# Kernel optimization log

Measured on AMD Instinct MI355X. Metric: run time of the kernel, lower is better.

Reference implementation:

```python
import jax, jax.numpy as jnp
import numpy as np

N_HEAD = 16
D_MODEL = 1024
HEAD_DIM = D_MODEL // N_HEAD


def setup_inputs() -> dict:
    key = jax.random.key(0)
    ks = jax.random.split(key, 12)
    B, S, D = 2, 2048, D_MODEL
    scale = 1.0 / np.sqrt(D)
    inp = {
        "q": jax.random.normal(ks[0], (B, S, D), jnp.float32),
        "k": jax.random.normal(ks[1], (B, S, D), jnp.float32),
        "v": jax.random.normal(ks[2], (B, S, D), jnp.float32),
        "mask": jax.random.randint(ks[3], (B, 1, S, S), 0, 2, jnp.int32),
        "wq": jax.random.normal(ks[4], (D, D), jnp.float32) * scale,
        "bq": jnp.zeros((D,), jnp.float32),
        "wk": jax.random.normal(ks[5], (D, D), jnp.float32) * scale,
        "bk": jnp.zeros((D,), jnp.float32),
        "wv": jax.random.normal(ks[6], (D, D), jnp.float32) * scale,
        "bv": jnp.zeros((D,), jnp.float32),
        "wo": jax.random.normal(ks[7], (D, D), jnp.float32) * scale,
        "bo": jnp.zeros((D,), jnp.float32),
    }
    return inp


def _split_heads(x):
    B, S, D = x.shape
    return x.reshape(B, S, N_HEAD, HEAD_DIM).transpose(0, 2, 1, 3)  # [B,H,S,Hd]


def reference(q, k, v, mask, wq, bq, wk, bk, wv, bv, wo, bo):
    _q = _split_heads(q @ wq + bq)
    _k = _split_heads(k @ wk + bk)
    _v = _split_heads(v @ wv + bv)
    inv = 1.0 / (jnp.sqrt(jnp.float32(HEAD_DIM)) + 1e-8)
    score = jnp.einsum("bhqd,bhkd->bhqk", _q, _k) * inv
    score = score + mask.astype(score.dtype) * (-1e9)
    attn = jax.nn.softmax(score, axis=-1)
    ctx = jnp.einsum("bhqk,bhkd->bhqd", attn, _v)
    B, H, S, Hd = ctx.shape
    ctx = ctx.transpose(0, 2, 1, 3).reshape(B, S, H * Hd)
    return ctx @ wo + bo  # dropout is identity (eval / drop_rate=0)
```

## Files before the change

### kernel.cpp

```cpp
#include <hip/hip_runtime.h>

typedef unsigned short u16;
typedef __bf16 bf16x8_t __attribute__((ext_vector_type(8)));
typedef float  f32x4_t  __attribute__((ext_vector_type(4)));
typedef u16    us8_t    __attribute__((ext_vector_type(8)));
typedef u16    us4_t    __attribute__((ext_vector_type(4)));

__device__ __forceinline__ u16 f2bf(float f) {
    __bf16 h = (__bf16)f;
    return __builtin_bit_cast(u16, h);
}
__device__ __forceinline__ bf16x8_t ld_bf8(const u16* p) {
    us8_t u = *(const us8_t*)p;
    return __builtin_bit_cast(bf16x8_t, u);
}
__device__ __forceinline__ f32x4_t mfma16(bf16x8_t a, bf16x8_t b, f32x4_t c) {
    return __builtin_amdgcn_mfma_f32_16x16x32_bf16(a, b, c, 0, 0, 0);
}
__device__ __forceinline__ float exp2_fast(float x) {
#if __has_builtin(__builtin_amdgcn_exp2f)
    return __builtin_amdgcn_exp2f(x);
#else
    return exp2f(x);
#endif
}

__device__ __forceinline__ void dma16(const u16* g, u16* l) {
#if __has_builtin(__builtin_amdgcn_global_load_lds)
    __builtin_amdgcn_global_load_lds((const __attribute__((address_space(1))) unsigned int*)(g),
                                     (__attribute__((address_space(3))) unsigned int*)(l), 16, 0, 0);
#else
    *(us8_t*)l = *(const us8_t*)g;
#endif
}

__global__ __launch_bounds__(256) void prep_kernel(
    const float* __restrict__ q, const float* __restrict__ k, const float* __restrict__ v,
    const int* __restrict__ mask,
    const float* __restrict__ w0, const float* __restrict__ w1,
    const float* __restrict__ w2, const float* __restrict__ w3,
    u16* __restrict__ Qc, u16* __restrict__ Kc, u16* __restrict__ Vc,
    u16* __restrict__ Wt, unsigned* __restrict__ mp)
{
    __shared__ u16 t[64][65];
    const int bid = blockIdx.x, tid = threadIdx.x;
    if (bid < 6144) {
        const int z = bid >> 11, x = bid & 2047;
        const float* src = (z == 0) ? q : (z == 1) ? k : v;
        u16* dst = (z == 0) ? Qc : (z == 1) ? Kc : Vc;
        const size_t i = ((size_t)x * 256 + tid) * 8;
        float4 a = *(const float4*)(src + i);
        float4 b = *(const float4*)(src + i + 4);
        us8_t w;
        w[0] = f2bf(a.x); w[1] = f2bf(a.y); w[2] = f2bf(a.z); w[3] = f2bf(a.w);
        w[4] = f2bf(b.x); w[5] = f2bf(b.y); w[6] = f2bf(b.z); w[7] = f2bf(b.w);
        *(us8_t*)(dst + i) = w;
    } else if (bid < 7168) {
        const int r2 = bid - 6144;
        const int z = r2 >> 8, rem = r2 & 255;
        const float* src = (z == 0) ? w0 : (z == 1) ? w1 : (z == 2) ? w2 : w3;
        u16* dst = Wt + (size_t)z * 1048576;
        const int bk = (rem & 15) * 64, bn = (rem >> 4) * 64;
        const int r = tid >> 2, c4 = tid & 3;
        for (int i = 0; i < 4; i++) {
            float4 vv = *(const float4*)(src + (size_t)(bk + r) * 1024 + bn + c4 * 16 + i * 4);
            t[r][c4 * 16 + i * 4 + 0] = f2bf(vv.x);
            t[r][c4 * 16 + i * 4 + 1] = f2bf(vv.y);
            t[r][c4 * 16 + i * 4 + 2] = f2bf(vv.z);
            t[r][c4 * 16 + i * 4 + 3] = f2bf(vv.w);
        }
        __syncthreads();
        for (int i = 0; i < 2; i++) {
            us8_t w;
            for (int j = 0; j < 8; j++) w[j] = t[c4 * 16 + i * 8 + j][r];
            *(us8_t*)(dst + (size_t)(bn + r) * 1024 + bk + c4 * 16 + i * 8) = w;
        }
    } else {
        const int w = (bid - 7168) * 256 + tid;
        const int* src = mask + (size_t)w * 32;
        unsigned bits = 0u;
        for (int i = 0; i < 32; i += 4) {
            int4 vv = *(const int4*)(src + i);
            bits |= (unsigned)(vv.x != 0) << (i + 0);
            bits |= (unsigned)(vv.y != 0) << (i + 1);
            bits |= (unsigned)(vv.z != 0) << (i + 2);
            bits |= (unsigned)(vv.w != 0) << (i + 3);
        }
        mp[w] = bits;
    }
}

__global__ __launch_bounds__(256) void qkv_gemm_kernel(
    const u16* __restrict__ Qc, const u16* __restrict__ Kc, const u16* __restrict__ Vc,
    const u16* __restrict__ Wt,
    const float* __restrict__ bq, const float* __restrict__ bk, const float* __restrict__ bv,
    u16* __restrict__ Qh, u16* __restrict__ Kh, u16* __restrict__ Vtt)
{
    __shared__ __align__(16) u16 As[4096];
    __shared__ __align__(16) u16 Bs[4096];
    const int z = blockIdx.z;
    const u16* A = (z == 0) ? Qc : (z == 1) ? Kc : Vc;
    const u16* W = Wt + (size_t)z * 1048576;
    const float* bias = (z == 0) ? bq : (z == 1) ? bk : bv;

    const int m0 = blockIdx.x * 128, n0 = blockIdx.y * 128;
    const int tid = threadIdx.x, lane = tid & 63, wave = tid >> 6;
    const int l15 = lane & 15, quad = lane >> 4;
    const int wm = (wave & 1) * 64, wn = (wave >> 1) * 64;
    const int srow = lane >> 2, scol = (lane & 3) * 8;

    const f32x4_t z4 = {0.f, 0.f, 0.f, 0.f};
    f32x4_t acc[4][4];
    for (int i = 0; i < 4; i++) for (int j = 0; j < 4; j++) acc[i][j] = z4;

    for (int k0 = 0; k0 < 1024; k0 += 32) {
        #pragma unroll
        for (int i = 0; i < 2; i++) {
            dma16(A + (size_t)(m0 + wave * 32 + i * 16 + srow) * 1024 + k0 + scol,
                  &As[wave * 1024 + i * 512 + lane * 8]);
            dma16(W + (size_t)(n0 + wave * 32 + i * 16 + srow) * 1024 + k0 + scol,
                  &Bs[wave * 1024 + i * 512 + lane * 8]);
        }
        __syncthreads();
        bf16x8_t af[4], bfr[4];
        #pragma unroll
        for (int i = 0; i < 4; i++) af[i] = ld_bf8(&As[(wm + i * 16 + l15) * 32 + quad * 8]);
        #pragma unroll
        for (int j = 0; j < 4; j++) bfr[j] = ld_bf8(&Bs[(wn + j * 16 + l15) * 32 + quad * 8]);
        #pragma unroll
        for (int i = 0; i < 4; i++)
            #pragma unroll
            for (int j = 0; j < 4; j++)
                acc[i][j] = mfma16(af[i], bfr[j], acc[i][j]);
        __syncthreads();
    }

    #pragma unroll
    for (int i = 0; i < 4; i++) {
        const int m = m0 + wm + i * 16 + quad * 4;
        #pragma unroll
        for (int j = 0; j < 4; j++) {
            const int gn = n0 + wn + j * 16 + l15;
            const float bb = bias[gn];
            const int h = gn >> 6, dh = gn & 63;
            if (z < 2) {
                u16* Y = z ? Kh : Qh;
                const int jc = dh >> 3, e = dh & 7;
                #pragma unroll
                for (int r = 0; r < 4; r++) {
                    const int mm = m + r;
                    const int b = mm >> 11, s = mm & 2047;
                    Y[((size_t)(b * 16 + h) * 2048 + s) * 64 + ((jc ^ (s & 7)) * 8) + e] =
                        f2bf(acc[i][j][r] + bb);
                }
            } else {
                const int b = m >> 11, sh = m & 2047, kt2 = sh >> 7, sl = sh & 127;
                const int poslow = ((sl >> 4) & 1) * 4;
                const int chunk = (sl >> 5) * 4 + ((sl >> 2) & 3);
                us4_t w4;
                #pragma unroll
                for (int r = 0; r < 4; r++) w4[r] = f2bf(acc[i][j][r] + bb);
                size_t off = (((size_t)(b * 16 + h) * 16 + kt2) * 8192)
                           + (size_t)dh * 128 + ((chunk ^ (dh & 7)) * 8) + poslow;
                *(us4_t*)&Vtt[off] = w4;
            }
        }
    }
}

__global__ __launch_bounds__(256) void out_gemm_kernel(
    const u16* __restrict__ X, const u16* __restrict__ Wt,
    const float* __restrict__ bias, float* __restrict__ Y)
{
    __shared__ __align__(16) u16 As[2048];
    __shared__ __align__(16) u16 Bs[4096];
    const int m0 = blockIdx.x * 64, n0 = blockIdx.y * 128;
    const int tid = threadIdx.x, lane = tid & 63, wave = tid >> 6;
    const int l15 = lane & 15, quad = lane >> 4;
    const int wm = (wave & 1) * 32, wn = (wave >> 1) * 64;
    const int srow = lane >> 2, scol = (lane & 3) * 8;

    const f32x4_t z4 = {0.f, 0.f, 0.f, 0.f};
    f32x4_t acc[2][4];
    for (int i = 0; i < 2; i++) for (int j = 0; j < 4; j++) acc[i][j] = z4;

    for (int k0 = 0; k0 < 1024; k0 += 32) {
        dma16(X + (size_t)(m0 + wave * 16 + srow) * 1024 + k0 + scol,
              &As[wave * 512 + lane * 8]);
        #pragma unroll
        for (int i = 0; i < 2; i++)
            dma16(Wt + (size_t)(n0 + wave * 32 + i * 16 + srow) * 1024 + k0 + scol,
                  &Bs[wave * 1024 + i * 512 + lane * 8]);
        __syncthreads();
        bf16x8_t af[2], bfr[4];
        #pragma unroll
        for (int i = 0; i < 2; i++) af[i] = ld_bf8(&As[(wm + i * 16 + l15) * 32 + quad * 8]);
        #pragma unroll
        for (int j = 0; j < 4; j++) bfr[j] = ld_bf8(&Bs[(wn + j * 16 + l15) * 32 + quad * 8]);
        #pragma unroll
        for (int i = 0; i < 2; i++)
            #pragma unroll
            for (int j = 0; j < 4; j++)
                acc[i][j] = mfma16(af[i], bfr[j], acc[i][j]);
        __syncthreads();
    }

    #pragma unroll
    for (int i = 0; i < 2; i++) {
        const int m = m0 + wm + i * 16 + quad * 4;
        #pragma unroll
        for (int j = 0; j < 4; j++) {
            const int gn = n0 + wn + j * 16 + l15;
            const float bb = bias[gn];
            #pragma unroll
            for (int r = 0; r < 4; r++)
                Y[(size_t)(m + r) * 1024 + gn] = acc[i][j][r] + bb;
        }
    }
}

__global__ __launch_bounds__(256, 4) void attn_kernel(
    const u16* __restrict__ Qh, const u16* __restrict__ Kh,
    const u16* __restrict__ Vtt, const unsigned* __restrict__ mp,
    u16* __restrict__ C)
{
    __shared__ __align__(16) u16 Ks[2][4096];
    __shared__ __align__(16) u16 Vs[2][4096];
    const int h = blockIdx.x, qb = blockIdx.y, b = blockIdx.z;
    const int tid = threadIdx.x, lane = tid & 63, wave = tid >> 6;
    const int l15 = lane & 15, quad = lane >> 4;
    const int q0 = qb * 64 + wave * 16;
    const int grow = b * 2048 + q0;
    const size_t headoff = (size_t)(b * 16 + h) * 131072;
    const u16* Qg = Qh + headoff;
    const u16* Kg = Kh + headoff;
    const u16* Vg = Vtt + headoff;

    bf16x8_t aq[2];
    #pragma unroll
    for (int ks = 0; ks < 2; ks++)
        aq[ks] = ld_bf8(Qg + (size_t)(q0 + l15) * 64 + (((ks * 4 + quad) ^ (l15 & 7)) * 8));

    us8_t ones_u;
    #pragma unroll
    for (int i = 0; i < 8; i++) ones_u[i] = 0x3F80;
    const bf16x8_t ones = __builtin_bit_cast(bf16x8_t, ones_u);

    const f32x4_t z4 = {0.f, 0.f, 0.f, 0.f};
    f32x4_t o[4];
    #pragma unroll
    for (int i = 0; i < 4; i++) o[i] = z4;
    f32x4_t osum = z4;

    const int swA = (quad ^ (l15 & 7)) * 8;
    const int swB = ((4 + quad) ^ (l15 & 7)) * 8;

    const unsigned* mrow = mp + (size_t)(b * 2048 + q0 + l15) * 64;

    auto stage = [&](int kt, int bs) {
        const u16* kg = Kg + kt * 4096 + wave * 1024;
        const u16* vg = Vg + (kt >> 1) * 8192 + (kt & 1) * 64;
        u16* kl = &Ks[bs][wave * 1024];
        u16* vl = &Vs[bs][wave * 1024];
        #pragma unroll
        for (int i = 0; i < 2; i++) {
            dma16(kg + i * 512 + lane * 8, kl + i * 512 + lane * 8);
            dma16(vg + (size_t)(wave * 16 + i * 8 + (lane >> 3)) * 128 + (lane & 7) * 8,
                  vl + i * 512 + lane * 8);
        }
    };

    stage(0, 0);

    for (int kt = 0; kt < 32; ++kt) {
        const int bs = kt & 1;
        __syncthreads();
        if (kt < 31) stage(kt + 1, bs ^ 1);

        const int2 mv = *(const int2*)(mrow + kt * 2);

        f32x4_t sc[4];
        __builtin_amdgcn_s_setprio(1);
        #pragma unroll
        for (int st = 0; st < 4; st++) {
            const u16* kp = &Ks[bs][(st * 16 + l15) * 64];
            bf16x8_t k0 = ld_bf8(kp + swA);
            bf16x8_t k1 = ld_bf8(kp + swB);
            sc[st] = mfma16(k1, aq[1], mfma16(k0, aq[0], z4));
        }
        __builtin_amdgcn_s_setprio(0);

        us8_t ap[2];
        #pragma unroll
        for (int st = 0; st < 4; st++) {
            const unsigned w = (st < 2) ? (unsigned)mv.x : (unsigned)mv.y;
            const int shbase = ((st & 1) << 4) + quad * 4;
            #pragma unroll
            for (int r = 0; r < 4; r++) {
                const bool msk = (w >> (shbase + r)) & 1u;
                const float t = fmaf(sc[st][r], 0.18033688011f, msk ? -1e5f : -17.312340491f);
                ap[st >> 1][((st & 1) << 2) + r] = f2bf(exp2_fast(t));
            }
        }

        __builtin_amdgcn_s_setprio(1);
        #pragma unroll
        for (int c = 0; c < 2; c++) {
            bf16x8_t a = __builtin_bit_cast(bf16x8_t, ap[c]);
            osum = mfma16(a, ones, osum);
            #pragma unroll
            for (int nt = 0; nt < 4; nt++) {
                bf16x8_t bv = ld_bf8(&Vs[bs][(nt * 16 + l15) * 64
                                             + (((c * 4 + quad) ^ (l15 & 7)) * 8)]);
                o[nt] = mfma16(a, bv, o[nt]);
            }
        }
        __builtin_amdgcn_s_setprio(0);
    }

    #pragma unroll
    for (int r = 0; r < 4; r++) {
        const float invl = 1.0f / osum[r];
        const int row = grow + quad * 4 + r;
        #pragma unroll
        for (int nt = 0; nt < 4; nt++)
            C[(size_t)row * 1024 + h * 64 + nt * 16 + l15] = f2bf(o[nt][r] * invl);
    }
}

extern "C" void kernel_launch(void* const* d_in, const int* in_sizes, int n_in,
                              void* d_out, int out_size, void* d_ws, size_t ws_size,
                              hipStream_t stream) {
    const float* q    = (const float*)d_in[0];
    const float* k    = (const float*)d_in[1];
    const float* v    = (const float*)d_in[2];
    const int*   mask = (const int*)d_in[3];
    const float* wq   = (const float*)d_in[4];
    const float* bq   = (const float*)d_in[5];
    const float* wk   = (const float*)d_in[6];
    const float* bk   = (const float*)d_in[7];
    const float* wv   = (const float*)d_in[8];
    const float* bv   = (const float*)d_in[9];
    const float* wo   = (const float*)d_in[10];
    const float* bo   = (const float*)d_in[11];
    float* out = (float*)d_out;

    char* ws = (char*)d_ws;
    const size_t MB = 1ull << 20;
    u16* Wt      = (u16*)(ws);
    u16* Qc      = (u16*)(ws + 8 * MB);
    u16* Kc      = (u16*)(ws + 16 * MB);
    u16* Vc      = (u16*)(ws + 24 * MB);
    u16* Qhh     = (u16*)(ws + 32 * MB);
    u16* Khh     = (u16*)(ws + 40 * MB);
    u16* Vtt     = (u16*)(ws + 48 * MB);
    u16* CT      = (u16*)(ws + 8 * MB);
    unsigned* mp = (unsigned*)(ws + 56 * MB);

    prep_kernel<<<dim3(8192), 256, 0, stream>>>(
        q, k, v, mask, wq, wk, wv, wo, Qc, Kc, Vc, Wt, mp);

    qkv_gemm_kernel<<<dim3(32, 8, 3), 256, 0, stream>>>(
        Qc, Kc, Vc, Wt, bq, bk, bv, Qhh, Khh, Vtt);

    attn_kernel<<<dim3(16, 32, 2), 256, 0, stream>>>(Qhh, Khh, Vtt, mp, CT);

    out_gemm_kernel<<<dim3(64, 8), 256, 0, stream>>>(CT, Wt + 3ull * 1048576, bo, out);
}
```

Before: 256.3 us.

## Double-buffer LDS tiles in QKV and output projection GEMMs

Both projection GEMM kernels now keep two LDS buffers per operand. The next k-tile is prefetched into the other buffer while MFMAs run on the current one, and the loop needs only one barrier per iteration instead of two. The aim is to hide global-to-LDS load latency behind compute and cut synchronisation stalls. The cost is twice the shared memory per block, which may lower occupancy.

```diff
diff --git a/kernel.cpp b/kernel.cpp
--- a/kernel.cpp
+++ b/kernel.cpp
@@ -96,8 +96,8 @@
     const float* __restrict__ bq, const float* __restrict__ bk, const float* __restrict__ bv,
     u16* __restrict__ Qh, u16* __restrict__ Kh, u16* __restrict__ Vtt)
 {
-    __shared__ __align__(16) u16 As[4096];
-    __shared__ __align__(16) u16 Bs[4096];
+    __shared__ __align__(16) u16 As[2][4096];
+    __shared__ __align__(16) u16 Bs[2][4096];
     const int z = blockIdx.z;
     const u16* A = (z == 0) ? Qc : (z == 1) ? Kc : Vc;
     const u16* W = Wt + (size_t)z * 1048576;
@@ -113,26 +113,34 @@
     f32x4_t acc[4][4];
     for (int i = 0; i < 4; i++) for (int j = 0; j < 4; j++) acc[i][j] = z4;
 
-    for (int k0 = 0; k0 < 1024; k0 += 32) {
+    auto stage = [&](int t, int bs) {
+        const int k0 = t * 32;
         #pragma unroll
         for (int i = 0; i < 2; i++) {
             dma16(A + (size_t)(m0 + wave * 32 + i * 16 + srow) * 1024 + k0 + scol,
-                  &As[wave * 1024 + i * 512 + lane * 8]);
+                  &As[bs][wave * 1024 + i * 512 + lane * 8]);
             dma16(W + (size_t)(n0 + wave * 32 + i * 16 + srow) * 1024 + k0 + scol,
-                  &Bs[wave * 1024 + i * 512 + lane * 8]);
-        }
+                  &Bs[bs][wave * 1024 + i * 512 + lane * 8]);
+        }
+    };
+
+    stage(0, 0);
+
+    for (int t = 0; t < 32; ++t) {
+        const int bs = t & 1;
         __syncthreads();
+        if (t < 31) stage(t + 1, bs ^ 1);
+
         bf16x8_t af[4], bfr[4];
         #pragma unroll
-        for (int i = 0; i < 4; i++) af[i] = ld_bf8(&As[(wm + i * 16 + l15) * 32 + quad * 8]);
-        #pragma unroll
-        for (int j = 0; j < 4; j++) bfr[j] = ld_bf8(&Bs[(wn + j * 16 + l15) * 32 + quad * 8]);
+        for (int i = 0; i < 4; i++) af[i] = ld_bf8(&As[bs][(wm + i * 16 + l15) * 32 + quad * 8]);
+        #pragma unroll
+        for (int j = 0; j < 4; j++) bfr[j] = ld_bf8(&Bs[bs][(wn + j * 16 + l15) * 32 + quad * 8]);
         #pragma unroll
         for (int i = 0; i < 4; i++)
             #pragma unroll
             for (int j = 0; j < 4; j++)
                 acc[i][j] = mfma16(af[i], bfr[j], acc[i][j]);
-        __syncthreads();
     }
 
     #pragma unroll
@@ -172,8 +180,8 @@
     const u16* __restrict__ X, const u16* __restrict__ Wt,
     const float* __restrict__ bias, float* __restrict__ Y)
 {
-    __shared__ __align__(16) u16 As[2048];
-    __shared__ __align__(16) u16 Bs[4096];
+    __shared__ __align__(16) u16 As[2][2048];
+    __shared__ __align__(16) u16 Bs[2][4096];
     const int m0 = blockIdx.x * 64, n0 = blockIdx.y * 128;
     const int tid = threadIdx.x, lane = tid & 63, wave = tid >> 6;
     const int l15 = lane & 15, quad = lane >> 4;
@@ -184,25 +192,33 @@
     f32x4_t acc[2][4];
     for (int i = 0; i < 2; i++) for (int j = 0; j < 4; j++) acc[i][j] = z4;
 
-    for (int k0 = 0; k0 < 1024; k0 += 32) {
+    auto stage = [&](int t, int bs) {
+        const int k0 = t * 32;
         dma16(X + (size_t)(m0 + wave * 16 + srow) * 1024 + k0 + scol,
-              &As[wave * 512 + lane * 8]);
+              &As[bs][wave * 512 + lane * 8]);
         #pragma unroll
         for (int i = 0; i < 2; i++)
             dma16(Wt + (size_t)(n0 + wave * 32 + i * 16 + srow) * 1024 + k0 + scol,
-                  &Bs[wave * 1024 + i * 512 + lane * 8]);
+                  &Bs[bs][wave * 1024 + i * 512 + lane * 8]);
+    };
+
+    stage(0, 0);
+
+    for (int t = 0; t < 32; ++t) {
+        const int bs = t & 1;
         __syncthreads();
+        if (t < 31) stage(t + 1, bs ^ 1);
+
         bf16x8_t af[2], bfr[4];
         #pragma unroll
-        for (int i = 0; i < 2; i++) af[i] = ld_bf8(&As[(wm + i * 16 + l15) * 32 + quad * 8]);
-        #pragma unroll
-        for (int j = 0; j < 4; j++) bfr[j] = ld_bf8(&Bs[(wn + j * 16 + l15) * 32 + quad * 8]);
+        for (int i = 0; i < 2; i++) af[i] = ld_bf8(&As[bs][(wm + i * 16 + l15) * 32 + quad * 8]);
+        #pragma unroll
+        for (int j = 0; j < 4; j++) bfr[j] = ld_bf8(&Bs[bs][(wn + j * 16 + l15) * 32 + quad * 8]);
         #pragma unroll
         for (int i = 0; i < 2; i++)
             #pragma unroll
             for (int j = 0; j < 4; j++)
                 acc[i][j] = mfma16(af[i], bfr[j], acc[i][j]);
-        __syncthreads();
     }
 
     #pragma unroll
```

After: 261.1 us. About the same (+1.9%).
